# Kernel tuning notes

Hardware: AMD Instinct MI355X
Metric: run time of the kernel (lower is better)

The kernel has to match this reference:

```python
import jax, jax.numpy as jnp
import numpy as np

N = 100000   # nodes (batched graph)
E = 1600000  # edges
G = 2048     # molecules in the batch
D_IN = 128
D_H = 128
MLP_H = 512


def setup_inputs() -> dict:
    key = jax.random.key(0)
    ks = jax.random.split(key, 20)

    def w(k, i, o):
        return (jax.random.normal(k, (i, o), jnp.float32) / np.sqrt(i)).astype(jnp.float32)

    feats = jax.random.normal(ks[0], (N, D_IN), jnp.float32)
    src = jax.random.randint(ks[1], (E,), 0, N)
    dst = jax.random.randint(ks[2], (E,), 0, N)
    graph_ids = jnp.sort(jax.random.randint(ks[3], (N,), 0, G))

    return {
        "feats": feats, "src": src, "dst": dst, "graph_ids": graph_ids,
        # 3 GraphConv layers
        "W0": w(ks[4], D_IN, D_H), "b0": jnp.zeros((D_H,), jnp.float32),
        "W1": w(ks[5], D_H, D_H),  "b1": jnp.zeros((D_H,), jnp.float32),
        "W2": w(ks[6], D_H, D_H),  "b2": jnp.zeros((D_H,), jnp.float32),
        # MLP head: D_H -> 512 -> 256 -> 1
        "Wm0": w(ks[7], D_H, MLP_H),       "bm0": jnp.zeros((MLP_H,), jnp.float32),
        "Wm1": w(ks[8], MLP_H, MLP_H // 2), "bm1": jnp.zeros((MLP_H // 2,), jnp.float32),
        "Wm2": w(ks[9], MLP_H // 2, 1),     "bm2": jnp.zeros((1,), jnp.float32),
    }


def reference(feats, src, dst, graph_ids, W0, b0, W1, b1, W2, b2,
              Wm0, bm0, Wm1, bm1, Wm2, bm2):
    ones_e = jnp.ones((E,), jnp.float32)
    # DGL GraphConv norm='both': D_out^{-1/2} on src, D_in^{-1/2} on dst; deg clamped to 1
    deg_out = jnp.maximum(jax.ops.segment_sum(ones_e, src, num_segments=N), 1.0)
    deg_in = jnp.maximum(jax.ops.segment_sum(ones_e, dst, num_segments=N), 1.0)
    inv_src = jax.lax.rsqrt(deg_out)[:, None]
    inv_dst = jax.lax.rsqrt(deg_in)[:, None]

    def gcn_layer(h, W, b):
        h = h * inv_src                                   # [N, D]
        m = jax.ops.segment_sum(h[src], dst, num_segments=N)  # gather-scatter over edges
        m = m * inv_dst
        return jax.nn.relu(jnp.dot(m, W) + b)

    h = gcn_layer(feats, W0, b0)
    h = gcn_layer(h, W1, b1)
    h = gcn_layer(h, W2, b2)

    # AvgPooling per graph
    counts = jnp.maximum(jax.ops.segment_sum(jnp.ones((N,), jnp.float32), graph_ids, num_segments=G), 1.0)
    emb = jax.ops.segment_sum(h, graph_ids, num_segments=G) / counts[:, None]  # [G, D_H]

    # MLP head (dropout = identity in eval)
    x = jax.nn.relu(jnp.dot(emb, Wm0) + bm0)
    x = jax.nn.relu(jnp.dot(x, Wm1) + bm1)
    return jnp.dot(x, Wm2) + bm2  # [G, 1]
```

## Files before the change

### kernel.cpp

```cpp
#include <hip/hip_runtime.h>


static inline int ceil_div(int a, int b){ return (a + b - 1) / b; }

#define B1 128
#define NBMAX 1024

__global__ __launch_bounds__(256) void bucket_count_kernel(
    const int* __restrict__ src, const int* __restrict__ dst,
    unsigned* __restrict__ cntA, unsigned* __restrict__ cntB,
    int E, int NB){
  __shared__ unsigned la[NBMAX], lb[NBMAX];
  int t = threadIdx.x;
  for (int i = t; i < NB; i += 256){ la[i] = 0u; lb[i] = 0u; }
  __syncthreads();
  int chunk = (E + B1 - 1) / B1;
  int e0 = blockIdx.x * chunk, e1 = min(e0 + chunk, E);
  for (int e = e0 + t; e < e1; e += 256){
    atomicAdd(&la[dst[e] >> 7], 1u);
    atomicAdd(&lb[src[e] >> 7], 1u);
  }
  __syncthreads();
  for (int i = t; i < NB; i += 256){
    cntA[(size_t)blockIdx.x * NB + i] = la[i];
    cntB[(size_t)blockIdx.x * NB + i] = lb[i];
  }
}

__global__ void scan_cols_kernel(unsigned* __restrict__ cntA, unsigned* __restrict__ cntB,
                                 unsigned* __restrict__ totals, int NB){
  int b = blockIdx.x * 256 + threadIdx.x;
  if (b >= NB) return;
  unsigned* cnt = blockIdx.y ? cntB : cntA;
  unsigned run = 0;
  for (int blk = 0; blk < B1; blk++){
    unsigned v = cnt[(size_t)blk * NB + b];
    cnt[(size_t)blk * NB + b] = run;
    run += v;
  }
  totals[(size_t)blockIdx.y * NB + b] = run;
}

__global__ void scan_base_kernel(const unsigned* __restrict__ totals,
                                 unsigned* __restrict__ baseA, unsigned* __restrict__ baseB,
                                 int NB, int E){
  __shared__ unsigned s[NBMAX];
  int t = threadIdx.x;
  for (int job = 0; job < 2; job++){
    unsigned* base = job ? baseB : baseA;
    unsigned x = (t < NB) ? totals[(size_t)job * NB + t] : 0u;
    s[t] = x;
    __syncthreads();
    for (int off = 1; off < NBMAX; off <<= 1){
      unsigned v = (t >= off) ? s[t - off] : 0u;
      __syncthreads();
      s[t] += v;
      __syncthreads();
    }
    if (t < NB) base[t] = s[t] - x;
    if (t == 0) base[NB] = (unsigned)E;
    __syncthreads();
  }
}

__global__ __launch_bounds__(256) void bucket_scatter_kernel(
    const int* __restrict__ src, const int* __restrict__ dst,
    const unsigned* __restrict__ cntA, const unsigned* __restrict__ cntB,
    const unsigned* __restrict__ baseA, const unsigned* __restrict__ baseB,
    unsigned* __restrict__ bpack_d, unsigned char* __restrict__ bsrc_s,
    int E, int NB){
  __shared__ unsigned curA[NBMAX], curB[NBMAX];
  int t = threadIdx.x;
  for (int i = t; i < NB; i += 256){
    curA[i] = baseA[i] + cntA[(size_t)blockIdx.x * NB + i];
    curB[i] = baseB[i] + cntB[(size_t)blockIdx.x * NB + i];
  }
  __syncthreads();
  int chunk = (E + B1 - 1) / B1;
  int e0 = blockIdx.x * chunk, e1 = min(e0 + chunk, E);
  for (int e = e0 + t; e < e1; e += 256){
    int s = src[e], d = dst[e];
    unsigned p = atomicAdd(&curA[d >> 7], 1u);
    bpack_d[p] = ((unsigned)(d & 127) << 17) | (unsigned)s;
    unsigned q = atomicAdd(&curB[s >> 7], 1u);
    bsrc_s[q] = (unsigned char)(s & 127);
  }
}

__global__ __launch_bounds__(256) void csr_finalize_kernel(
    const unsigned* __restrict__ bpack_d, const unsigned* __restrict__ baseA,
    int* __restrict__ row_ptr, float* __restrict__ inv_dst, int* __restrict__ col,
    int N, int E, int NB){
  __shared__ unsigned cnt[128];
  __shared__ unsigned scn[128];
  int b = blockIdx.x, t = threadIdx.x;
  int node0 = b << 7;
  int nn = min(128, N - node0);
  int e0 = (int)baseA[b], e1 = (int)baseA[b + 1];
  if (t < 128) cnt[t] = 0u;
  __syncthreads();
  for (int e = e0 + t; e < e1; e += 256)
    atomicAdd(&cnt[(bpack_d[e] >> 17) & 127u], 1u);
  __syncthreads();
  unsigned mycnt = (t < 128) ? cnt[t] : 0u;
  if (t < 128) scn[t] = mycnt;
  __syncthreads();
  for (int off = 1; off < 128; off <<= 1){
    unsigned v = (t < 128 && t >= off) ? scn[t - off] : 0u;
    __syncthreads();
    if (t < 128) scn[t] += v;
    __syncthreads();
  }
  if (t < nn){
    unsigned excl = scn[t] - mycnt;
    row_ptr[node0 + t] = e0 + (int)excl;
    unsigned c = mycnt < 1u ? 1u : mycnt;
    inv_dst[node0 + t] = rsqrtf((float)c);
    cnt[t] = (unsigned)e0 + excl;
  }
  if (b == NB - 1 && t == 0) row_ptr[N] = E;
  __syncthreads();
  for (int e = e0 + t; e < e1; e += 256){
    unsigned v = bpack_d[e];
    unsigned p = atomicAdd(&cnt[(v >> 17) & 127u], 1u);
    col[p] = (int)(v & 0x1FFFFu);
  }
}

__global__ __launch_bounds__(256) void degout_finalize_kernel(
    const unsigned char* __restrict__ bsrc_s, const unsigned* __restrict__ baseB,
    float* __restrict__ inv_src, int N){
  __shared__ unsigned cnt[128];
  int b = blockIdx.x, t = threadIdx.x;
  int node0 = b << 7;
  int nn = min(128, N - node0);
  int e0 = (int)baseB[b], e1 = (int)baseB[b + 1];
  if (t < 128) cnt[t] = 0u;
  __syncthreads();
  for (int e = e0 + t; e < e1; e += 256)
    atomicAdd(&cnt[bsrc_s[e]], 1u);
  __syncthreads();
  if (t < nn){
    unsigned c = cnt[t] < 1u ? 1u : cnt[t];
    inv_src[node0 + t] = rsqrtf((float)c);
  }
}

__global__ void scale_rows_kernel(const float* __restrict__ in, const float* __restrict__ sc,
                                  float* __restrict__ out, int n4){
  int i = blockIdx.x*blockDim.x + threadIdx.x;
  if (i < n4){
    float4 v = ((const float4*)in)[i];
    float s = sc[i >> 5];
    v.x *= s; v.y *= s; v.z *= s; v.w *= s;
    ((float4*)out)[i] = v;
  }
}

__global__ __launch_bounds__(256) void csr_agg_kernel(
    const int* __restrict__ row_ptr, const int* __restrict__ col,
    const float* __restrict__ hs, float* __restrict__ agg, int N){
  int node = (int)((blockIdx.x*256u + threadIdx.x) >> 5);
  int lane = threadIdx.x & 31;
  if (node >= N) return;
  int r0 = row_ptr[node];
  int r1 = row_ptr[node+1];
  float4 a0 = make_float4(0.f,0.f,0.f,0.f);
  float4 a1 = make_float4(0.f,0.f,0.f,0.f);
  float4 a2 = make_float4(0.f,0.f,0.f,0.f);
  float4 a3 = make_float4(0.f,0.f,0.f,0.f);
  int e = r0;
  for (; e + 3 < r1; e += 4){
    int s0 = col[e], s1 = col[e+1], s2 = col[e+2], s3 = col[e+3];
    float4 v0 = ((const float4*)(hs + (size_t)s0*128))[lane];
    float4 v1 = ((const float4*)(hs + (size_t)s1*128))[lane];
    float4 v2 = ((const float4*)(hs + (size_t)s2*128))[lane];
    float4 v3 = ((const float4*)(hs + (size_t)s3*128))[lane];
    a0.x += v0.x; a0.y += v0.y; a0.z += v0.z; a0.w += v0.w;
    a1.x += v1.x; a1.y += v1.y; a1.z += v1.z; a1.w += v1.w;
    a2.x += v2.x; a2.y += v2.y; a2.z += v2.z; a2.w += v2.w;
    a3.x += v3.x; a3.y += v3.y; a3.z += v3.z; a3.w += v3.w;
  }
  for (; e < r1; e++){
    int s0 = col[e];
    float4 v0 = ((const float4*)(hs + (size_t)s0*128))[lane];
    a0.x += v0.x; a0.y += v0.y; a0.z += v0.z; a0.w += v0.w;
  }
  float4 r;
  r.x = (a0.x + a1.x) + (a2.x + a3.x);
  r.y = (a0.y + a1.y) + (a2.y + a3.y);
  r.z = (a0.z + a1.z) + (a2.z + a3.z);
  r.w = (a0.w + a1.w) + (a2.w + a3.w);
  ((float4*)(agg + (size_t)node*128))[lane] = r;
}

__global__ __launch_bounds__(256) void gemm_kernel(
    const float* __restrict__ A, const float* __restrict__ W,
    const float* __restrict__ bias, const float* __restrict__ row_scale,
    const float* __restrict__ out_scale, float* __restrict__ out,
    int M, int K, int Ncols, int do_relu){
  __shared__ float As[32][68];
  __shared__ float Bs[32][128];

  const int tid = threadIdx.x;
  const int tx = tid & 31;
  const int ty = tid >> 5;
  const int row0 = blockIdx.x * 64;
  const int col0 = blockIdx.y * 128;

  float acc[8][4];
  #pragma unroll
  for (int i = 0; i < 8; i++)
    #pragma unroll
    for (int j = 0; j < 4; j++) acc[i][j] = 0.f;

  for (int kb = 0; kb < K; kb += 32){
    #pragma unroll
    for (int i = 0; i < 2; i++){
      int flat = i*256 + tid;
      int m = flat >> 3, k4 = (flat & 7) << 2;
      int gm = row0 + m;
      float4 v = make_float4(0.f, 0.f, 0.f, 0.f);
      if (gm < M){
        v = *(const float4*)(A + (size_t)gm*K + kb + k4);
        if (row_scale){ float s = row_scale[gm]; v.x*=s; v.y*=s; v.z*=s; v.w*=s; }
      }
      As[k4+0][m] = v.x; As[k4+1][m] = v.y; As[k4+2][m] = v.z; As[k4+3][m] = v.w;
    }
    #pragma unroll
    for (int i = 0; i < 4; i++){
      int flat = i*256 + tid;
      int k = flat >> 5, j4 = (flat & 31) << 2;
      float4 v = *(const float4*)(W + (size_t)(kb + k)*Ncols + col0 + j4);
      *(float4*)&Bs[k][j4] = v;
    }
    __syncthreads();
    #pragma unroll
    for (int k = 0; k < 32; k++){
      float4 b = *(const float4*)&Bs[k][tx << 2];
      float a[8];
      #pragma unroll
      for (int i = 0; i < 8; i++) a[i] = As[k][ty*8 + i];
      #pragma unroll
      for (int i = 0; i < 8; i++){
        acc[i][0] = fmaf(a[i], b.x, acc[i][0]);
        acc[i][1] = fmaf(a[i], b.y, acc[i][1]);
        acc[i][2] = fmaf(a[i], b.z, acc[i][2]);
        acc[i][3] = fmaf(a[i], b.w, acc[i][3]);
      }
    }
    __syncthreads();
  }

  float4 bi = *(const float4*)(bias + col0 + (tx << 2));
  #pragma unroll
  for (int i = 0; i < 8; i++){
    int gm = row0 + ty*8 + i;
    if (gm < M){
      float4 v;
      v.x = acc[i][0] + bi.x; v.y = acc[i][1] + bi.y;
      v.z = acc[i][2] + bi.z; v.w = acc[i][3] + bi.w;
      if (do_relu){
        v.x = fmaxf(v.x, 0.f); v.y = fmaxf(v.y, 0.f);
        v.z = fmaxf(v.z, 0.f); v.w = fmaxf(v.w, 0.f);
      }
      if (out_scale){ float s = out_scale[gm]; v.x*=s; v.y*=s; v.z*=s; v.w*=s; }
      *(float4*)(out + (size_t)gm*Ncols + col0 + (tx << 2)) = v;
    }
  }
}

__global__ void pool_kernel(const float* __restrict__ h, const int* __restrict__ gid,
                            float* __restrict__ emb, int N, int G){
  int g = blockIdx.x;
  int lane = threadIdx.x;
  int lo = 0, hi = N;
  while (lo < hi){ int mid = (lo + hi) >> 1; if (gid[mid] < g) lo = mid + 1; else hi = mid; }
  int start = lo;
  hi = N;
  while (lo < hi){ int mid = (lo + hi) >> 1; if (gid[mid] <= g) lo = mid + 1; else hi = mid; }
  int end = lo;
  float ax = 0.f, ay = 0.f;
  for (int n = start; n < end; n++){
    float2 v = ((const float2*)(h + (size_t)n*128))[lane];
    ax += v.x; ay += v.y;
  }
  int c = end - start; if (c < 1) c = 1;
  float invc = 1.0f / (float)c;
  float2 r; r.x = ax * invc; r.y = ay * invc;
  ((float2*)(emb + (size_t)g*128))[lane] = r;
}

__global__ void final_dot_kernel(const float* __restrict__ x, const float* __restrict__ w,
                                 const float* __restrict__ b, float* __restrict__ out, int G){
  int idx = blockIdx.x*blockDim.x + threadIdx.x;
  int g = idx >> 6, lane = idx & 63;
  if (g >= G) return;
  float4 xv = ((const float4*)(x + (size_t)g*256))[lane];
  float4 wv = ((const float4*)w)[lane];
  float s = xv.x*wv.x + xv.y*wv.y + xv.z*wv.z + xv.w*wv.w;
  for (int off = 32; off > 0; off >>= 1) s += __shfl_down(s, off);
  if (lane == 0) out[g] = s + b[0];
}

extern "C" void kernel_launch(void* const* d_in, const int* in_sizes, int n_in,
                              void* d_out, int out_size, void* d_ws, size_t ws_size,
                              hipStream_t stream){
  const float* feats = (const float*)d_in[0];
  const int*   src   = (const int*)d_in[1];
  const int*   dst   = (const int*)d_in[2];
  const int*   gid   = (const int*)d_in[3];
  const float* W0 = (const float*)d_in[4];   const float* b0 = (const float*)d_in[5];
  const float* W1 = (const float*)d_in[6];   const float* b1 = (const float*)d_in[7];
  const float* W2 = (const float*)d_in[8];   const float* b2 = (const float*)d_in[9];
  const float* Wm0 = (const float*)d_in[10]; const float* bm0 = (const float*)d_in[11];
  const float* Wm1 = (const float*)d_in[12]; const float* bm1 = (const float*)d_in[13];
  const float* Wm2 = (const float*)d_in[14]; const float* bm2 = (const float*)d_in[15];
  float* out = (float*)d_out;

  const int E   = in_sizes[1];
  const int N   = in_sizes[3];
  const int G   = out_size;
  const int MH  = in_sizes[11];
  const int MH2 = in_sizes[13];
  const int NB  = ceil_div(N, 128);

  char* ws = (char*)d_ws;
  size_t off = 0;
  auto carve = [&](size_t bytes) -> char* {
    off = (off + 255) & ~(size_t)255;
    char* p = ws + off; off += bytes; return p;
  };
  float* inv_src = (float*)carve((size_t)N*4);
  float* inv_dst = (float*)carve((size_t)N*4);
  int* row_ptr = (int*)carve((size_t)(N+1)*4);
  int* col     = (int*)carve((size_t)E*4);
  float* hs  = (float*)carve((size_t)N*128*4);
  float* agg = (float*)carve((size_t)N*128*4);
  float* emb = (float*)carve((size_t)G*128*4);
  float* x1  = (float*)carve((size_t)G*MH*4);
  float* x2  = (float*)carve((size_t)G*MH2*4);

  unsigned* T = (unsigned*)agg;
  unsigned* cntA   = T;
  unsigned* cntB   = cntA + (size_t)B1*NB;
  unsigned* totals = cntB + (size_t)B1*NB;
  unsigned* baseA  = totals + 2*(size_t)NB;
  unsigned* baseB  = baseA + (NB+1);
  unsigned* bpack_d = baseB + (NB+1);
  unsigned char* bsrc_s = (unsigned char*)(bpack_d + E);

  bucket_count_kernel<<<B1, 256, 0, stream>>>(src, dst, cntA, cntB, E, NB);
  scan_cols_kernel<<<dim3(ceil_div(NB,256), 2), 256, 0, stream>>>(cntA, cntB, totals, NB);
  scan_base_kernel<<<1, NBMAX, 0, stream>>>(totals, baseA, baseB, NB, E);
  bucket_scatter_kernel<<<B1, 256, 0, stream>>>(src, dst, cntA, cntB, baseA, baseB,
                                                bpack_d, bsrc_s, E, NB);
  csr_finalize_kernel<<<NB, 256, 0, stream>>>(bpack_d, baseA, row_ptr, inv_dst, col, N, E, NB);
  degout_finalize_kernel<<<NB, 256, 0, stream>>>(bsrc_s, baseB, inv_src, N);
  scale_rows_kernel<<<ceil_div(N*32,256), 256, 0, stream>>>(feats, inv_src, hs, N*32);

  const int agg_blocks = ceil_div(N*32, 256);
  dim3 ggrid(ceil_div(N,64), 1);
  csr_agg_kernel<<<agg_blocks, 256, 0, stream>>>(row_ptr, col, hs, agg, N);
  gemm_kernel<<<ggrid, 256, 0, stream>>>(agg, W0, b0, inv_dst, inv_src, hs, N, 128, 128, 1);
  csr_agg_kernel<<<agg_blocks, 256, 0, stream>>>(row_ptr, col, hs, agg, N);
  gemm_kernel<<<ggrid, 256, 0, stream>>>(agg, W1, b1, inv_dst, inv_src, hs, N, 128, 128, 1);
  csr_agg_kernel<<<agg_blocks, 256, 0, stream>>>(row_ptr, col, hs, agg, N);
  gemm_kernel<<<ggrid, 256, 0, stream>>>(agg, W2, b2, inv_dst, nullptr, hs, N, 128, 128, 1);
  pool_kernel<<<G, 64, 0, stream>>>(hs, gid, emb, N, G);
  gemm_kernel<<<dim3(ceil_div(G,64), MH/128),  256, 0, stream>>>(emb, Wm0, bm0, nullptr, nullptr, x1, G, 128, MH, 1);
  gemm_kernel<<<dim3(ceil_div(G,64), MH2/128), 256, 0, stream>>>(x1, Wm1, bm1, nullptr, nullptr, x2, G, MH, MH2, 1);
  final_dot_kernel<<<ceil_div(G*64,256), 256, 0, stream>>>(x2, Wm2, bm2, out, G);
}
```

Baseline: 814.6 us.

## Use split-bf16 MFMA for the GCN layer GEMMs

Replaces the FP32 SIMT tiled GEMM for the three 128x128 GCN layer transforms with a matrix-core kernel. It uses the bf16 hi/lo split trick with three MFMA products to keep near-FP32 accuracy. A small prep kernel splits and transposes each weight matrix into bf16 hi/lo parts, and the row scaling, bias, ReLU and output scaling stay fused in the kernel. B fragments are read straight from global/L2 without LDS staging, and the last block loads A rows past M without clamping.

```diff
diff --git a/kernel.cpp b/kernel.cpp
--- a/kernel.cpp
+++ b/kernel.cpp
@@ -5,6 +5,9 @@
 
 #define B1 128
 #define NBMAX 1024
+
+typedef __bf16 bf16x8 __attribute__((ext_vector_type(8)));
+typedef float  f32x4  __attribute__((ext_vector_type(4)));
 
 __global__ __launch_bounds__(256) void bucket_count_kernel(
     const int* __restrict__ src, const int* __restrict__ dst,
@@ -194,6 +197,94 @@
   ((float4*)(agg + (size_t)node*128))[lane] = r;
 }
 
+__global__ void wprep_kernel(const float* __restrict__ W,
+                             __bf16* __restrict__ Whi, __bf16* __restrict__ Wlo){
+  int idx = blockIdx.x*256 + threadIdx.x;
+  if (idx >= 128*128) return;
+  int k = idx >> 7, n = idx & 127;
+  float w = W[idx];
+  __bf16 h = (__bf16)w;
+  __bf16 l = (__bf16)(w - (float)h);
+  Whi[n*128 + k] = h;
+  Wlo[n*128 + k] = l;
+}
+
+__global__ __launch_bounds__(256) void mfma_gemm_kernel(
+    const float* __restrict__ A,
+    const __bf16* __restrict__ Whi, const __bf16* __restrict__ Wlo,
+    const float* __restrict__ bias, const float* __restrict__ row_scale,
+    const float* __restrict__ out_scale, float* __restrict__ out, int M){
+  const int tid  = threadIdx.x;
+  const int wv   = tid >> 6;
+  const int lane = tid & 63;
+  const int q    = lane >> 4;
+  const int mn   = lane & 15;
+  const int row0 = blockIdx.x*128 + wv*32;
+
+  f32x4 acc[2][8];
+  #pragma unroll
+  for (int mt = 0; mt < 2; mt++)
+    #pragma unroll
+    for (int nt = 0; nt < 8; nt++)
+      acc[mt][nt] = (f32x4){0.f,0.f,0.f,0.f};
+
+  float rs[2];
+  #pragma unroll
+  for (int mt = 0; mt < 2; mt++){
+    int ridx = row0 + mt*16 + mn;
+    if (ridx >= M) ridx = M - 1;
+    rs[mt] = row_scale ? row_scale[ridx] : 1.f;
+  }
+
+  #pragma unroll
+  for (int kc = 0; kc < 4; kc++){
+    bf16x8 ah[2], al[2];
+    #pragma unroll
+    for (int mt = 0; mt < 2; mt++){
+      const float* ap = A + (size_t)(row0 + mt*16 + mn)*128 + kc*32 + q*8;
+      float4 x0 = *(const float4*)ap;
+      float4 x1 = *(const float4*)(ap + 4);
+      float v[8] = {x0.x, x0.y, x0.z, x0.w, x1.x, x1.y, x1.z, x1.w};
+      #pragma unroll
+      for (int j = 0; j < 8; j++){
+        float s = v[j] * rs[mt];
+        __bf16 h = (__bf16)s;
+        ah[mt][j] = h;
+        al[mt][j] = (__bf16)(s - (float)h);
+      }
+    }
+    #pragma unroll
+    for (int nt = 0; nt < 8; nt++){
+      size_t boff = (size_t)(nt*16 + mn)*128 + kc*32 + q*8;
+      bf16x8 bh = *(const bf16x8*)(Whi + boff);
+      bf16x8 bl = *(const bf16x8*)(Wlo + boff);
+      #pragma unroll
+      for (int mt = 0; mt < 2; mt++){
+        acc[mt][nt] = __builtin_amdgcn_mfma_f32_16x16x32_bf16(al[mt], bh, acc[mt][nt], 0, 0, 0);
+        acc[mt][nt] = __builtin_amdgcn_mfma_f32_16x16x32_bf16(ah[mt], bl, acc[mt][nt], 0, 0, 0);
+        acc[mt][nt] = __builtin_amdgcn_mfma_f32_16x16x32_bf16(ah[mt], bh, acc[mt][nt], 0, 0, 0);
+      }
+    }
+  }
+
+  #pragma unroll
+  for (int mt = 0; mt < 2; mt++){
+    #pragma unroll
+    for (int r = 0; r < 4; r++){
+      int gm = row0 + mt*16 + q*4 + r;
+      if (gm < M){
+        float osc = out_scale ? out_scale[gm] : 1.f;
+        #pragma unroll
+        for (int nt = 0; nt < 8; nt++){
+          float v = acc[mt][nt][r] + bias[nt*16 + mn];
+          v = fmaxf(v, 0.f) * osc;
+          out[(size_t)gm*128 + nt*16 + mn] = v;
+        }
+      }
+    }
+  }
+}
+
 __global__ __launch_bounds__(256) void gemm_kernel(
     const float* __restrict__ A, const float* __restrict__ W,
     const float* __restrict__ bias, const float* __restrict__ row_scale,
@@ -335,6 +426,8 @@
   float* inv_dst = (float*)carve((size_t)N*4);
   int* row_ptr = (int*)carve((size_t)(N+1)*4);
   int* col     = (int*)carve((size_t)E*4);
+  __bf16* Wsp[6];
+  for (int i = 0; i < 6; i++) Wsp[i] = (__bf16*)carve(128*128*2);
   float* hs  = (float*)carve((size_t)N*128*4);
   float* agg = (float*)carve((size_t)N*128*4);
   float* emb = (float*)carve((size_t)G*128*4);
@@ -357,16 +450,19 @@
                                                 bpack_d, bsrc_s, E, NB);
   csr_finalize_kernel<<<NB, 256, 0, stream>>>(bpack_d, baseA, row_ptr, inv_dst, col, N, E, NB);
   degout_finalize_kernel<<<NB, 256, 0, stream>>>(bsrc_s, baseB, inv_src, N);
+  wprep_kernel<<<64, 256, 0, stream>>>(W0, Wsp[0], Wsp[1]);
+  wprep_kernel<<<64, 256, 0, stream>>>(W1, Wsp[2], Wsp[3]);
+  wprep_kernel<<<64, 256, 0, stream>>>(W2, Wsp[4], Wsp[5]);
   scale_rows_kernel<<<ceil_div(N*32,256), 256, 0, stream>>>(feats, inv_src, hs, N*32);
 
   const int agg_blocks = ceil_div(N*32, 256);
-  dim3 ggrid(ceil_div(N,64), 1);
+  const int ggrid = ceil_div(N, 128);
   csr_agg_kernel<<<agg_blocks, 256, 0, stream>>>(row_ptr, col, hs, agg, N);
-  gemm_kernel<<<ggrid, 256, 0, stream>>>(agg, W0, b0, inv_dst, inv_src, hs, N, 128, 128, 1);
+  mfma_gemm_kernel<<<ggrid, 256, 0, stream>>>(agg, Wsp[0], Wsp[1], b0, inv_dst, inv_src, hs, N);
   csr_agg_kernel<<<agg_blocks, 256, 0, stream>>>(row_ptr, col, hs, agg, N);
-  gemm_kernel<<<ggrid, 256, 0, stream>>>(agg, W1, b1, inv_dst, inv_src, hs, N, 128, 128, 1);
+  mfma_gemm_kernel<<<ggrid, 256, 0, stream>>>(agg, Wsp[2], Wsp[3], b1, inv_dst, inv_src, hs, N);
   csr_agg_kernel<<<agg_blocks, 256, 0, stream>>>(row_ptr, col, hs, agg, N);
-  gemm_kernel<<<ggrid, 256, 0, stream>>>(agg, W2, b2, inv_dst, nullptr, hs, N, 128, 128, 1);
+  mfma_gemm_kernel<<<ggrid, 256, 0, stream>>>(agg, Wsp[4], Wsp[5], b2, inv_dst, nullptr, hs, N);
   pool_kernel<<<G, 64, 0, stream>>>(hs, gid, emb, N, G);
   gemm_kernel<<<dim3(ceil_div(G,64), MH/128),  256, 0, stream>>>(emb, Wm0, bm0, nullptr, nullptr, x1, G, 128, MH, 1);
   gemm_kernel<<<dim3(ceil_div(G,64), MH2/128), 256, 0, stream>>>(x1, Wm1, bm1, nullptr, nullptr, x2, G, MH, MH2, 1);
```

Result: no change. 804.6 us (-1.2%).
